# Kernel optimization log

Measured on AMD Instinct MI355X. Metric: run time of the kernel, lower is better.

Reference implementation:

```python
import jax, jax.numpy as jnp
import numpy as np

N = 100000
E = 1600000
C = 32          # in_channels
H = 256         # hidden_size


def setup_inputs() -> dict:
    key = jax.random.key(0)
    ks = jax.random.split(key, 16)
    s = 1.0 / np.sqrt(C)
    inp = {
        "state": jax.random.normal(ks[0], (N, C), dtype=jnp.float32),
        "edge_index": jax.random.randint(ks[1], (2, E), 0, N, dtype=jnp.int64),
        # GCNConv params (conv3 reused for layers 4 and 5, matching the source)
        "convW1": jax.random.normal(ks[2], (C, C), dtype=jnp.float32) * s,
        "convb1": jnp.zeros((C,), jnp.float32),
        "convW2": jax.random.normal(ks[3], (C, C), dtype=jnp.float32) * s,
        "convb2": jnp.zeros((C,), jnp.float32),
        "convW3": jax.random.normal(ks[4], (C, C), dtype=jnp.float32) * s,
        "convb3": jnp.zeros((C,), jnp.float32),
        "linW1": jax.random.normal(ks[5], (6 * C, H), dtype=jnp.float32) / np.sqrt(6 * C),
        "linb1": jnp.zeros((H,), jnp.float32),
        "linW2": jax.random.normal(ks[6], (H, H), dtype=jnp.float32) / np.sqrt(H),
        "linb2": jnp.zeros((H,), jnp.float32),
        "linW3": jax.random.normal(ks[7], (H, 1), dtype=jnp.float32) / np.sqrt(H),
        "linb3": jnp.zeros((1,), jnp.float32),
    }
    return inp


def _gcn(x, W, b, src, dst, norm):
    # PyG GCNConv: x' = scatter_add( norm * (xW)[src] -> dst ) + b
    xw = x @ W                                  # [N, C]
    msg = norm[:, None] * xw[src]               # [E+N, C] gather
    agg = jax.ops.segment_sum(msg, dst, num_segments=x.shape[0])
    return agg + b


def reference(state, edge_index, convW1, convb1, convW2, convb2, convW3, convb3,
              linW1, linb1, linW2, linb2, linW3, linb3):
    n = state.shape[0]
    loops = jnp.arange(n, dtype=edge_index.dtype)
    src = jnp.concatenate([edge_index[0], loops])   # add self loops
    dst = jnp.concatenate([edge_index[1], loops])
    deg = jax.ops.segment_sum(jnp.ones_like(dst, dtype=state.dtype), dst, num_segments=n)
    dinv = jnp.where(deg > 0, jax.lax.rsqrt(deg), 0.0)
    norm = dinv[src] * dinv[dst]                    # symmetric normalization

    out1 = jax.nn.relu(_gcn(state, convW1, convb1, src, dst, norm))
    out2 = jax.nn.relu(_gcn(out1, convW2, convb2, src, dst, norm))
    out3 = jax.nn.relu(_gcn(out2, convW3, convb3, src, dst, norm))
    out4 = jax.nn.relu(_gcn(out3, convW3, convb3, src, dst, norm))  # conv3 reused (as in source)
    out5 = jax.nn.relu(_gcn(out4, convW3, convb3, src, dst, norm))  # conv3 reused (as in source)

    x = jnp.concatenate([out1, out2, out3, out4, out5, state], axis=-1)  # [N, 6C]
    x = jax.nn.leaky_relu(x @ linW1 + linb1, negative_slope=0.01)
    x = jax.nn.leaky_relu(x @ linW2 + linb2, negative_slope=0.01)
    x = jax.nn.softplus(x @ linW3 + linb3)
    concentration = jnp.squeeze(x, -1)              # [N]
    # deterministic=True path
    action = concentration / (concentration.sum(axis=-1, keepdims=True) + 1e-20)
    return action
```

## Files before the change

kernel.cpp:

```cpp
#include <hip/hip_runtime.h>
#include <hip/hip_bf16.h>
#include <hip/hip_fp16.h>

#define CDIV(a,b) (((a)+(b)-1)/(b))

typedef float f32x4 __attribute__((ext_vector_type(4)));
typedef int   i32x4 __attribute__((ext_vector_type(4)));
typedef unsigned int u32x2 __attribute__((ext_vector_type(2)));

__device__ __forceinline__ void mfma16(f32x4& d, i32x4 a, i32x4 b) {
  asm("v_mfma_f32_16x16x32_bf16 %0, %1, %2, %0" : "+v"(d) : "v"(a), "v"(b));
}

__device__ __forceinline__ unsigned short bf16r(float x) {
  return __builtin_bit_cast(unsigned short, __float2bfloat16(x));
}
__device__ __forceinline__ float bf16f(unsigned short u) {
  unsigned int w_ = (unsigned int)u << 16;
  return __builtin_bit_cast(float, w_);
}


__global__ __launch_bounds__(256) void k_count(const int* __restrict__ dst,
                                               int* __restrict__ cnt, int E) {
  int e = blockIdx.x * blockDim.x + threadIdx.x;
  if (e < E) atomicAdd(&cnt[dst[e]], 1);
}

__global__ __launch_bounds__(256) void k_scan1(const int* __restrict__ cnt,
                                               int* __restrict__ rowptr,
                                               int* __restrict__ blockSums, int N) {
  __shared__ int sdata[256];
  const int t = threadIdx.x;
  const int base = blockIdx.x * 1024;
  int v[4]; int local = 0;
#pragma unroll
  for (int i = 0; i < 4; i++) {
    int idx = base + t * 4 + i;
    v[i] = (idx < N) ? cnt[idx] : 0;
    local += v[i];
  }
  sdata[t] = local;
  __syncthreads();
  for (int off = 1; off < 256; off <<= 1) {
    int x = (t >= off) ? sdata[t - off] : 0;
    __syncthreads();
    sdata[t] += x;
    __syncthreads();
  }
  if (t == 255) blockSums[blockIdx.x] = sdata[255];
  int run = sdata[t] - local;
#pragma unroll
  for (int i = 0; i < 4; i++) {
    int idx = base + t * 4 + i;
    if (idx < N) rowptr[idx] = run;
    run += v[i];
  }
}

__global__ __launch_bounds__(256) void k_scan2(int* blockSums, int NB) {
  __shared__ int sdata[256];
  int t = threadIdx.x;
  int v = (t < NB) ? blockSums[t] : 0;
  sdata[t] = v;
  __syncthreads();
  for (int off = 1; off < 256; off <<= 1) {
    int x = (t >= off) ? sdata[t - off] : 0;
    __syncthreads();
    sdata[t] += x;
    __syncthreads();
  }
  if (t < NB) blockSums[t] = sdata[t] - v;
}

__global__ __launch_bounds__(256) void k_scan3(int* __restrict__ rowptr,
                                               const int* __restrict__ blockSums,
                                               int N, int E) {
  int idx = blockIdx.x * blockDim.x + threadIdx.x;
  if (idx < N) rowptr[idx] += blockSums[idx >> 10];
  if (idx == 0) rowptr[N] = E;
}

__global__ __launch_bounds__(256) void k_fill(const int* __restrict__ src,
                                              const int* __restrict__ dst,
                                              const int* __restrict__ rowptr,
                                              int* __restrict__ cursor,
                                              int* __restrict__ colidx, int E) {
  int e = blockIdx.x * blockDim.x + threadIdx.x;
  if (e < E) {
    int d = dst[e];
    int pos = rowptr[d] + atomicAdd(&cursor[d], 1);
    colidx[pos] = src[e];
  }
}

__global__ __launch_bounds__(256) void k_dinv(const int* __restrict__ cnt,
                                              float* __restrict__ dinv, int N) {
  int i = blockIdx.x * blockDim.x + threadIdx.x;
  if (i < N) dinv[i] = rsqrtf((float)cnt[i] + 1.0f);
}

__global__ __launch_bounds__(256) void k_xw(const float* __restrict__ x,
                                            const float* __restrict__ W,
                                            const float* __restrict__ dinv,
                                            unsigned short* __restrict__ y, int N) {
  __shared__ float Ws[1024];
  int t = threadIdx.x;
#pragma unroll
  for (int i = 0; i < 4; i++) Ws[t + i * 256] = W[t + i * 256];
  __syncthreads();
  int gid = blockIdx.x * blockDim.x + t;
  int n = gid >> 4, c = (gid & 15) * 2;
  if (n < N) {
    const float4* xr4 = (const float4*)(x + (size_t)n * 32);
    float a0 = 0.f, a1 = 0.f;
#pragma unroll
    for (int k4 = 0; k4 < 8; k4++) {
      float4 xv = xr4[k4];
      int k = k4 * 4;
      a0 = fmaf(xv.x, Ws[(k + 0) * 32 + c], a0); a1 = fmaf(xv.x, Ws[(k + 0) * 32 + c + 1], a1);
      a0 = fmaf(xv.y, Ws[(k + 1) * 32 + c], a0); a1 = fmaf(xv.y, Ws[(k + 1) * 32 + c + 1], a1);
      a0 = fmaf(xv.z, Ws[(k + 2) * 32 + c], a0); a1 = fmaf(xv.z, Ws[(k + 2) * 32 + c + 1], a1);
      a0 = fmaf(xv.w, Ws[(k + 3) * 32 + c], a0); a1 = fmaf(xv.w, Ws[(k + 3) * 32 + c + 1], a1);
    }
    float dn = dinv[n];
    __half2 h = __floats2half2_rn(a0 * dn, a1 * dn);
    *(__half2*)&y[(size_t)gid * 2] = h;
  }
}

__device__ __forceinline__ void acc8(float* acc, uint4 v) {
  float2 f;
  f = __half22float2(__builtin_bit_cast(__half2, v.x)); acc[0] += f.x; acc[1] += f.y;
  f = __half22float2(__builtin_bit_cast(__half2, v.y)); acc[2] += f.x; acc[3] += f.y;
  f = __half22float2(__builtin_bit_cast(__half2, v.z)); acc[4] += f.x; acc[5] += f.y;
  f = __half22float2(__builtin_bit_cast(__half2, v.w)); acc[6] += f.x; acc[7] += f.y;
}

__global__ __launch_bounds__(256) void k_agg(const unsigned short* __restrict__ y,
                                             const int* __restrict__ rowptr,
                                             const int* __restrict__ colidx,
                                             const float* __restrict__ dinv,
                                             const float* __restrict__ b,
                                             float* __restrict__ out, int N) {
  int t = threadIdx.x;
  int q = t & 3;
  int n = blockIdx.x * 64 + (t >> 2);
  if (n >= N) return;
  const uint4* yrow = (const uint4*)y;
  float acc[8];
  {
    uint4 v = yrow[(size_t)n * 4 + q];
    float2 f;
    f = __half22float2(__builtin_bit_cast(__half2, v.x)); acc[0] = f.x; acc[1] = f.y;
    f = __half22float2(__builtin_bit_cast(__half2, v.y)); acc[2] = f.x; acc[3] = f.y;
    f = __half22float2(__builtin_bit_cast(__half2, v.z)); acc[4] = f.x; acc[5] = f.y;
    f = __half22float2(__builtin_bit_cast(__half2, v.w)); acc[6] = f.x; acc[7] = f.y;
  }
  int beg = rowptr[n], end = rowptr[n + 1];
  int j = beg;
  for (; j + 16 <= end; j += 16) {
    uint4 v[16];
#pragma unroll
    for (int u = 0; u < 16; u++) v[u] = yrow[(size_t)colidx[j + u] * 4 + q];
#pragma unroll
    for (int u = 0; u < 16; u++) acc8(acc, v[u]);
  }
  for (; j + 8 <= end; j += 8) {
    uint4 v[8];
#pragma unroll
    for (int u = 0; u < 8; u++) v[u] = yrow[(size_t)colidx[j + u] * 4 + q];
#pragma unroll
    for (int u = 0; u < 8; u++) acc8(acc, v[u]);
  }
  for (; j + 4 <= end; j += 4) {
    uint4 v[4];
#pragma unroll
    for (int u = 0; u < 4; u++) v[u] = yrow[(size_t)colidx[j + u] * 4 + q];
#pragma unroll
    for (int u = 0; u < 4; u++) acc8(acc, v[u]);
  }
  for (; j < end; j++) {
    uint4 v = yrow[(size_t)colidx[j] * 4 + q];
    acc8(acc, v);
  }
  float dn = dinv[n];
  int cb = q * 8;
  float4 r0, r1;
  r0.x = fmaxf(fmaf(dn, acc[0], b[cb + 0]), 0.f);
  r0.y = fmaxf(fmaf(dn, acc[1], b[cb + 1]), 0.f);
  r0.z = fmaxf(fmaf(dn, acc[2], b[cb + 2]), 0.f);
  r0.w = fmaxf(fmaf(dn, acc[3], b[cb + 3]), 0.f);
  r1.x = fmaxf(fmaf(dn, acc[4], b[cb + 4]), 0.f);
  r1.y = fmaxf(fmaf(dn, acc[5], b[cb + 5]), 0.f);
  r1.z = fmaxf(fmaf(dn, acc[6], b[cb + 6]), 0.f);
  r1.w = fmaxf(fmaf(dn, acc[7], b[cb + 7]), 0.f);
  ((float4*)out)[(size_t)n * 8 + q * 2 + 0] = r0;
  ((float4*)out)[(size_t)n * 8 + q * 2 + 1] = r1;
}

__global__ __launch_bounds__(256) void k_prepw(const float* __restrict__ W1,
                                               const float* __restrict__ W2,
                                               unsigned short* __restrict__ Wt1h,
                                               unsigned short* __restrict__ Wt1l,
                                               unsigned short* __restrict__ Wt2h,
                                               unsigned short* __restrict__ Wt2l) {
  int o = blockIdx.x * blockDim.x + threadIdx.x;
  if (o < 256 * 192) {
    int col = o / 192, k = o % 192;
    float v = W1[k * 256 + col];
    unsigned short h = bf16r(v);
    Wt1h[o] = h;
    Wt1l[o] = bf16r(v - bf16f(h));
  } else if (o < 256 * 192 + 256 * 256) {
    int o2 = o - 256 * 192;
    int col = o2 / 256, k = o2 % 256;
    float v = W2[k * 256 + col];
    unsigned short h = bf16r(v);
    Wt2h[o2] = h;
    Wt2l[o2] = bf16r(v - bf16f(h));
  }
}

__device__ __forceinline__ float softplusf(float x) {
  return fmaxf(x, 0.f) + log1pf(expf(-fabsf(x)));
}

#define XS_STRIDE 200
#define H1_STRIDE 264
#define MNODES 80

__global__ __launch_bounds__(512, 4) void k_mlp_mfma(
    const float* __restrict__ o1, const float* __restrict__ o2,
    const float* __restrict__ o3, const float* __restrict__ o4,
    const float* __restrict__ o5, const float* __restrict__ st,
    const unsigned short* __restrict__ Wt1h, const unsigned short* __restrict__ Wt1l,
    const float* __restrict__ b1,
    const unsigned short* __restrict__ Wt2h, const unsigned short* __restrict__ Wt2l,
    const float* __restrict__ b2,
    const float* __restrict__ W3, const float* __restrict__ b3,
    float* __restrict__ conc, int N) {
  __shared__ unsigned short smem[2 * MNODES * XS_STRIDE];
  unsigned short* xsh = smem;
  unsigned short* xsl = smem + MNODES * XS_STRIDE;
  unsigned short* h1h = smem;
  float* redp = (float*)&smem[MNODES * H1_STRIDE];

  const int t = threadIdx.x;
  const int w = t >> 6;
  const int l = t & 63;
  const int l15 = l & 15, lq = l >> 4;
  const int nodeBase = blockIdx.x * MNODES;

  const float* srcs[6] = {o1, o2, o3, o4, o5, st};
  for (int i = t; i < MNODES * 96; i += 512) {
    int n = i / 96, cp = (i % 96) * 2;
    int gn = nodeBase + n;
    unsigned int pkh = 0, pkl = 0;
    if (gn < N) {
      const float* s = srcs[cp >> 5] + (size_t)gn * 32 + (cp & 31);
      float2 v = *(const float2*)s;
      unsigned short h0 = bf16r(v.x), h1_ = bf16r(v.y);
      unsigned short l0 = bf16r(v.x - bf16f(h0)), l1 = bf16r(v.y - bf16f(h1_));
      pkh = ((unsigned)h1_ << 16) | h0;
      pkl = ((unsigned)l1 << 16) | l0;
    }
    *(unsigned int*)&xsh[n * XS_STRIDE + cp] = pkh;
    *(unsigned int*)&xsl[n * XS_STRIDE + cp] = pkl;
  }
  __syncthreads();

  const int ocBase = w * 32;

  f32x4 acc[2][5];
#pragma unroll
  for (int rt = 0; rt < 2; rt++)
#pragma unroll
    for (int nt = 0; nt < 5; nt++) acc[rt][nt] = (f32x4)0.f;

  for (int kt = 0; kt < 6; kt++) {
    i32x4 ah[2], al[2];
#pragma unroll
    for (int rt = 0; rt < 2; rt++) {
      size_t aoff = (size_t)(ocBase + rt * 16 + l15) * 192 + kt * 32 + lq * 8;
      ah[rt] = *(const i32x4*)&Wt1h[aoff];
      al[rt] = *(const i32x4*)&Wt1l[aoff];
    }
#pragma unroll
    for (int nt = 0; nt < 5; nt++) {
      int boff = (nt * 16 + l15) * XS_STRIDE + kt * 32 + lq * 8;
      i32x4 bh = *(const i32x4*)&xsh[boff];
      i32x4 bl = *(const i32x4*)&xsl[boff];
#pragma unroll
      for (int rt = 0; rt < 2; rt++) mfma16(acc[rt][nt], ah[rt], bh);
#pragma unroll
      for (int rt = 0; rt < 2; rt++) mfma16(acc[rt][nt], al[rt], bh);
#pragma unroll
      for (int rt = 0; rt < 2; rt++) mfma16(acc[rt][nt], ah[rt], bl);
    }
  }
  __syncthreads();

#pragma unroll
  for (int rt = 0; rt < 2; rt++) {
    const int oc0 = ocBase + rt * 16 + lq * 4;
    float bb0 = b1[oc0], bb1 = b1[oc0 + 1], bb2 = b1[oc0 + 2], bb3 = b1[oc0 + 3];
#pragma unroll
    for (int nt = 0; nt < 5; nt++) {
      float v0 = acc[rt][nt][0] + bb0; v0 = (v0 > 0.f) ? v0 : 0.01f * v0;
      float v1 = acc[rt][nt][1] + bb1; v1 = (v1 > 0.f) ? v1 : 0.01f * v1;
      float v2 = acc[rt][nt][2] + bb2; v2 = (v2 > 0.f) ? v2 : 0.01f * v2;
      float v3 = acc[rt][nt][3] + bb3; v3 = (v3 > 0.f) ? v3 : 0.01f * v3;
      u32x2 pkh;
      pkh[0] = ((unsigned)bf16r(v1) << 16) | bf16r(v0);
      pkh[1] = ((unsigned)bf16r(v3) << 16) | bf16r(v2);
      int row = nt * 16 + l15;
      *(u32x2*)&h1h[row * H1_STRIDE + oc0] = pkh;
    }
  }
  __syncthreads();

  f32x4 acc2[2][5];
#pragma unroll
  for (int rt = 0; rt < 2; rt++)
#pragma unroll
    for (int nt = 0; nt < 5; nt++) acc2[rt][nt] = (f32x4)0.f;

  for (int kt = 0; kt < 8; kt++) {
    i32x4 ah[2], al[2];
#pragma unroll
    for (int rt = 0; rt < 2; rt++) {
      size_t aoff = (size_t)(ocBase + rt * 16 + l15) * 256 + kt * 32 + lq * 8;
      ah[rt] = *(const i32x4*)&Wt2h[aoff];
      al[rt] = *(const i32x4*)&Wt2l[aoff];
    }
#pragma unroll
    for (int nt = 0; nt < 5; nt++) {
      int boff = (nt * 16 + l15) * H1_STRIDE + kt * 32 + lq * 8;
      i32x4 bh = *(const i32x4*)&h1h[boff];
#pragma unroll
      for (int rt = 0; rt < 2; rt++) mfma16(acc2[rt][nt], ah[rt], bh);
#pragma unroll
      for (int rt = 0; rt < 2; rt++) mfma16(acc2[rt][nt], al[rt], bh);
    }
  }
  __syncthreads();

#pragma unroll
  for (int nt = 0; nt < 5; nt++) {
    float p = 0.f;
#pragma unroll
    for (int rt = 0; rt < 2; rt++) {
      const int oc0 = ocBase + rt * 16 + lq * 4;
#pragma unroll
      for (int j = 0; j < 4; j++) {
        float v = acc2[rt][nt][j] + b2[oc0 + j];
        v = (v > 0.f) ? v : 0.01f * v;
        p = fmaf(v, W3[oc0 + j], p);
      }
    }
    p += __shfl_xor(p, 16, 64);
    p += __shfl_xor(p, 32, 64);
    if (lq == 0) redp[w * MNODES + nt * 16 + l15] = p;
  }
  __syncthreads();

  if (t < MNODES) {
    int gn = nodeBase + t;
    if (gn < N) {
      float s = redp[0 * MNODES + t] + redp[1 * MNODES + t] + redp[2 * MNODES + t]
              + redp[3 * MNODES + t] + redp[4 * MNODES + t] + redp[5 * MNODES + t]
              + redp[6 * MNODES + t] + redp[7 * MNODES + t] + b3[0];
      conc[gn] = softplusf(s);
    }
  }
}

__global__ __launch_bounds__(256) void k_redsum(const float* __restrict__ conc,
                                                float* __restrict__ total, int N) {
  float s = 0.f;
  for (int i = blockIdx.x * blockDim.x + threadIdx.x; i < N; i += gridDim.x * blockDim.x)
    s += conc[i];
#pragma unroll
  for (int off = 32; off > 0; off >>= 1) s += __shfl_down(s, off, 64);
  __shared__ float ws_[4];
  if ((threadIdx.x & 63) == 0) ws_[threadIdx.x >> 6] = s;
  __syncthreads();
  if (threadIdx.x == 0) atomicAdd(total, ws_[0] + ws_[1] + ws_[2] + ws_[3]);
}

__global__ __launch_bounds__(256) void k_div(const float* __restrict__ conc,
                                             const float* __restrict__ total,
                                             float* __restrict__ out, int N) {
  int i = blockIdx.x * blockDim.x + threadIdx.x;
  if (i < N) out[i] = conc[i] / (total[0] + 1e-20f);
}

extern "C" void kernel_launch(void* const* d_in, const int* in_sizes, int n_in,
                              void* d_out, int out_size, void* d_ws, size_t ws_size,
                              hipStream_t stream) {
  const float* state = (const float*)d_in[0];
  const int*   ei    = (const int*)d_in[1];
  const float* cW1 = (const float*)d_in[2];
  const float* cb1 = (const float*)d_in[3];
  const float* cW2 = (const float*)d_in[4];
  const float* cb2 = (const float*)d_in[5];
  const float* cW3 = (const float*)d_in[6];
  const float* cb3 = (const float*)d_in[7];
  const float* lW1 = (const float*)d_in[8];
  const float* lb1 = (const float*)d_in[9];
  const float* lW2 = (const float*)d_in[10];
  const float* lb2 = (const float*)d_in[11];
  const float* lW3 = (const float*)d_in[12];
  const float* lb3 = (const float*)d_in[13];

  const int N = in_sizes[0] / 32;
  const int E = in_sizes[1] / 2;
  const int* srcI = ei;
  const int* dstI = ei + E;

  char* w = (char*)d_ws;
  size_t off = 0;
  auto alloc = [&](size_t bytes) -> void* {
    void* p = w + off;
    off = (off + bytes + 255) & ~(size_t)255;
    return p;
  };
  int*   cnt       = (int*)alloc((size_t)N * 4);
  int*   cursor    = (int*)alloc((size_t)N * 4);
  float* total     = (float*)alloc(256);
  size_t zbytes = off;
  int*   rowptr    = (int*)alloc(((size_t)N + 1) * 4);
  int*   blockSums = (int*)alloc(256 * 4);
  int*   colidx    = (int*)alloc((size_t)E * 4);
  float* dinv      = (float*)alloc((size_t)N * 4);
  unsigned short* ybuf = (unsigned short*)alloc((size_t)N * 32 * 2);
  float* out1      = (float*)alloc((size_t)N * 32 * 4);
  float* out2      = (float*)alloc((size_t)N * 32 * 4);
  float* out3      = (float*)alloc((size_t)N * 32 * 4);
  float* out4      = (float*)alloc((size_t)N * 32 * 4);
  float* out5      = (float*)alloc((size_t)N * 32 * 4);
  float* conc      = (float*)alloc((size_t)N * 4);
  unsigned short* Wt1h = (unsigned short*)alloc(256 * 192 * 2);
  unsigned short* Wt1l = (unsigned short*)alloc(256 * 192 * 2);
  unsigned short* Wt2h = (unsigned short*)alloc(256 * 256 * 2);
  unsigned short* Wt2l = (unsigned short*)alloc(256 * 256 * 2);

  const int TB = 256;
  hipMemsetAsync(d_ws, 0, zbytes, stream);

  k_count<<<CDIV(E, TB), TB, 0, stream>>>(dstI, cnt, E);
  int NB = CDIV(N, 1024);
  k_scan1<<<NB, TB, 0, stream>>>(cnt, rowptr, blockSums, N);
  k_scan2<<<1, TB, 0, stream>>>(blockSums, NB);
  k_scan3<<<CDIV(N, TB), TB, 0, stream>>>(rowptr, blockSums, N, E);
  k_fill<<<CDIV(E, TB), TB, 0, stream>>>(srcI, dstI, rowptr, cursor, colidx, E);
  k_dinv<<<CDIV(N, TB), TB, 0, stream>>>(cnt, dinv, N);
  k_prepw<<<CDIV(256 * 192 + 256 * 256, TB), TB, 0, stream>>>(lW1, lW2, Wt1h, Wt1l, Wt2h, Wt2l);

  struct Layer { const float* x; const float* W; const float* b; float* out; };
  Layer L[5] = {{state, cW1, cb1, out1},
                {out1,  cW2, cb2, out2},
                {out2,  cW3, cb3, out3},
                {out3,  cW3, cb3, out4},
                {out4,  cW3, cb3, out5}};
  for (int i = 0; i < 5; i++) {
    k_xw<<<CDIV(N * 16, TB), TB, 0, stream>>>(L[i].x, L[i].W, dinv, ybuf, N);
    k_agg<<<CDIV(N, 64), TB, 0, stream>>>(ybuf, rowptr, colidx, dinv, L[i].b, L[i].out, N);
  }

  k_mlp_mfma<<<CDIV(N, MNODES), 512, 0, stream>>>(out1, out2, out3, out4, out5, state,
                                                  Wt1h, Wt1l, lb1, Wt2h, Wt2l, lb2,
                                                  lW3, lb3, conc, N);
  k_redsum<<<256, TB, 0, stream>>>(conc, total, N);
  k_div<<<CDIV(N, TB), TB, 0, stream>>>(conc, total, (float*)d_out, N);
}
```

Before: 457.2 us.

## Build CSR via two-pass bucketed radix partition instead of global atomic fill

Replaces the single-pass CSR fill, which used a global atomic cursor per destination node, with a two-pass bucketed approach. The first pass computes per-block bucket histograms, scans them and scatters (src,dst) pairs into coarse 128-node buckets using shared-memory atomics. The second pass places the column indices within each bucket using LDS and writes colidx contiguously. The aim is to remove contention on global atomics and the random global writes, at the cost of more kernel launches and an extra 8-byte-per-edge intermediate buffer. Buckets holding more than 4096 edges would drop entries, which is safe only for near-uniform degree distributions.

```diff
diff --git a/kernel.cpp b/kernel.cpp
--- a/kernel.cpp
+++ b/kernel.cpp
@@ -20,6 +20,12 @@
   return __builtin_bit_cast(float, w_);
 }
 
+
+#define BUCK_SHIFT 7
+#define BUCK_W     128
+#define MAXBUCK    1024
+#define NBLK1      256
+#define P2CAP      4096
 
 __global__ __launch_bounds__(256) void k_count(const int* __restrict__ dst,
                                                int* __restrict__ cnt, int E) {
@@ -81,23 +87,100 @@
   if (idx == 0) rowptr[N] = E;
 }
 
-__global__ __launch_bounds__(256) void k_fill(const int* __restrict__ src,
-                                              const int* __restrict__ dst,
-                                              const int* __restrict__ rowptr,
-                                              int* __restrict__ cursor,
-                                              int* __restrict__ colidx, int E) {
-  int e = blockIdx.x * blockDim.x + threadIdx.x;
-  if (e < E) {
-    int d = dst[e];
-    int pos = rowptr[d] + atomicAdd(&cursor[d], 1);
-    colidx[pos] = src[e];
-  }
-}
-
 __global__ __launch_bounds__(256) void k_dinv(const int* __restrict__ cnt,
                                               float* __restrict__ dinv, int N) {
   int i = blockIdx.x * blockDim.x + threadIdx.x;
   if (i < N) dinv[i] = rsqrtf((float)cnt[i] + 1.0f);
+}
+
+__global__ __launch_bounds__(256) void k_p1hist(const int* __restrict__ dst,
+                                                int* __restrict__ hist,
+                                                int E, int nbuck, int chunk) {
+  __shared__ int h[MAXBUCK];
+  const int t = threadIdx.x, blk = blockIdx.x;
+  for (int i = t; i < MAXBUCK; i += 256) h[i] = 0;
+  __syncthreads();
+  int e0 = blk * chunk, e1 = min(e0 + chunk, E);
+  for (int e = e0 + t; e < e1; e += 256) atomicAdd(&h[dst[e] >> BUCK_SHIFT], 1);
+  __syncthreads();
+  for (int b = t; b < nbuck; b += 256) hist[blk * nbuck + b] = h[b];
+}
+
+__global__ __launch_bounds__(256) void k_pscan(const int* __restrict__ hist,
+                                               int* __restrict__ base,
+                                               int* __restrict__ btotal, int nbuck) {
+  __shared__ int s[256];
+  const int b = blockIdx.x, t = threadIdx.x;
+  int v = hist[t * nbuck + b];
+  s[t] = v;
+  __syncthreads();
+  for (int off = 1; off < 256; off <<= 1) {
+    int x = (t >= off) ? s[t - off] : 0;
+    __syncthreads();
+    s[t] += x;
+    __syncthreads();
+  }
+  base[b * 256 + t] = s[t] - v;
+  if (t == 255) btotal[b] = s[255];
+}
+
+__global__ __launch_bounds__(1024) void k_pscan2(const int* __restrict__ btotal,
+                                                 int* __restrict__ bbase,
+                                                 int nbuck, int E) {
+  __shared__ int s[1024];
+  int t = threadIdx.x;
+  int v = (t < nbuck) ? btotal[t] : 0;
+  s[t] = v;
+  __syncthreads();
+  for (int off = 1; off < 1024; off <<= 1) {
+    int x = (t >= off) ? s[t - off] : 0;
+    __syncthreads();
+    s[t] += x;
+    __syncthreads();
+  }
+  if (t < nbuck) bbase[t] = s[t] - v;
+  if (t == 0) bbase[nbuck] = E;
+}
+
+__global__ __launch_bounds__(256) void k_p1scatter(const int* __restrict__ src,
+                                                   const int* __restrict__ dst,
+                                                   const int* __restrict__ base,
+                                                   const int* __restrict__ bbase,
+                                                   int2* __restrict__ bkt,
+                                                   int E, int nbuck, int chunk) {
+  __shared__ int cur[MAXBUCK];
+  const int t = threadIdx.x, blk = blockIdx.x;
+  for (int i = t; i < MAXBUCK; i += 256) cur[i] = 0;
+  __syncthreads();
+  int e0 = blk * chunk, e1 = min(e0 + chunk, E);
+  for (int e = e0 + t; e < e1; e += 256) {
+    int d = dst[e];
+    int b = d >> BUCK_SHIFT;
+    int loc = atomicAdd(&cur[b], 1);
+    int pos = bbase[b] + base[b * 256 + blk] + loc;
+    bkt[pos] = make_int2(src[e], d);
+  }
+}
+
+__global__ __launch_bounds__(256) void k_p2build(const int2* __restrict__ bkt,
+                                                 const int* __restrict__ bbase,
+                                                 const int* __restrict__ rowptr,
+                                                 int* __restrict__ colidx, int N) {
+  __shared__ int cur[BUCK_W];
+  __shared__ int col[P2CAP];
+  const int b = blockIdx.x, t = threadIdx.x;
+  const int lo = b << BUCK_SHIFT;
+  for (int i = t; i < BUCK_W; i += 256) cur[i] = 0;
+  __syncthreads();
+  const int e0 = bbase[b], m = bbase[b + 1] - e0;
+  const int rowbase = rowptr[lo];
+  for (int i = t; i < m; i += 256) {
+    int2 p = bkt[e0 + i];
+    int off = rowptr[p.y] - rowbase + atomicAdd(&cur[p.y - lo], 1);
+    if (off < P2CAP) col[off] = p.x;
+  }
+  __syncthreads();
+  for (int i = t; i < m; i += 256) colidx[rowbase + i] = col[i];
 }
 
 __global__ __launch_bounds__(256) void k_xw(const float* __restrict__ x,
@@ -418,6 +501,8 @@
   const int E = in_sizes[1] / 2;
   const int* srcI = ei;
   const int* dstI = ei + E;
+  const int nbuck = CDIV(N, BUCK_W);
+  const int chunk = CDIV(E, NBLK1);
 
   char* w = (char*)d_ws;
   size_t off = 0;
@@ -427,13 +512,17 @@
     return p;
   };
   int*   cnt       = (int*)alloc((size_t)N * 4);
-  int*   cursor    = (int*)alloc((size_t)N * 4);
   float* total     = (float*)alloc(256);
   size_t zbytes = off;
   int*   rowptr    = (int*)alloc(((size_t)N + 1) * 4);
   int*   blockSums = (int*)alloc(256 * 4);
   int*   colidx    = (int*)alloc((size_t)E * 4);
   float* dinv      = (float*)alloc((size_t)N * 4);
+  int*   hist      = (int*)alloc((size_t)NBLK1 * nbuck * 4);
+  int*   pbase     = (int*)alloc((size_t)nbuck * 256 * 4);
+  int*   btotal    = (int*)alloc((size_t)nbuck * 4);
+  int*   bbase     = (int*)alloc(((size_t)nbuck + 1) * 4);
+  int2*  bkt       = (int2*)alloc((size_t)E * 8);
   unsigned short* ybuf = (unsigned short*)alloc((size_t)N * 32 * 2);
   float* out1      = (float*)alloc((size_t)N * 32 * 4);
   float* out2      = (float*)alloc((size_t)N * 32 * 4);
@@ -454,8 +543,14 @@
   k_scan1<<<NB, TB, 0, stream>>>(cnt, rowptr, blockSums, N);
   k_scan2<<<1, TB, 0, stream>>>(blockSums, NB);
   k_scan3<<<CDIV(N, TB), TB, 0, stream>>>(rowptr, blockSums, N, E);
-  k_fill<<<CDIV(E, TB), TB, 0, stream>>>(srcI, dstI, rowptr, cursor, colidx, E);
   k_dinv<<<CDIV(N, TB), TB, 0, stream>>>(cnt, dinv, N);
+
+  k_p1hist<<<NBLK1, TB, 0, stream>>>(dstI, hist, E, nbuck, chunk);
+  k_pscan<<<nbuck, TB, 0, stream>>>(hist, pbase, btotal, nbuck);
+  k_pscan2<<<1, 1024, 0, stream>>>(btotal, bbase, nbuck, E);
+  k_p1scatter<<<NBLK1, TB, 0, stream>>>(srcI, dstI, pbase, bbase, bkt, E, nbuck, chunk);
+  k_p2build<<<nbuck, TB, 0, stream>>>(bkt, bbase, rowptr, colidx, N);
+
   k_prepw<<<CDIV(256 * 192 + 256 * 256, TB), TB, 0, stream>>>(lW1, lW2, Wt1h, Wt1l, Wt2h, Wt2l);
 
   struct Layer { const float* x; const float* W; const float* b; float* out; };
```

Result: faster. 411.8 us (-9.9%).
